# Performance work log

Hardware: AMD Instinct MI355X
Metric: run time of the kernel (lower is better)

Reference implementation:

```python
import jax, jax.numpy as jnp
import numpy as np
from jax import lax

D = 4            # shift radius
NSHIFT = 2 * D + 1  # 9 shifts per axis -> 81 total


def setup_inputs() -> dict:
    key = jax.random.key(0)
    k1, k2, k3, k4, k5, k6 = jax.random.split(key, 6)
    B, C, H, W = 4, 256, 64, 128
    R = 16  # reduction ratio
    feat1 = jax.random.normal(k1, (B, C, H, W), dtype=jnp.float32)
    feat2 = jax.random.normal(k2, (B, C, H, W), dtype=jnp.float32)
    # ca_conv1: Conv2d(C, C//R, 1) -> weight [C//R, C], bias [C//R]
    w1 = jax.random.normal(k3, (C // R, C), dtype=jnp.float32) * (1.0 / np.sqrt(C))
    b1 = jax.random.normal(k4, (C // R,), dtype=jnp.float32) * 0.01
    # ca_conv2: Conv2d(C//R, C, 1) -> weight [C, C//R], bias [C]
    w2 = jax.random.normal(k5, (C, C // R), dtype=jnp.float32) * (1.0 / np.sqrt(C // R))
    b2 = jax.random.normal(k6, (C,), dtype=jnp.float32) * 0.01
    return {"feat1": feat1, "feat2": feat2, "w1": w1, "b1": b1, "w2": w2, "b2": b2}


def reference(feat1, feat2, w1, b1, w2, b2):
    B, C, H, W = feat1.shape
    # zero-pad feat2 spatially by D on each side (matches F.pad constant 0)
    feat2p = jnp.pad(feat2, ((0, 0), (0, 0), (D, D), (D, D)))

    def one_shift(carry, idx):
        i = idx // NSHIFT
        j = idx % NSHIFT
        f2 = lax.dynamic_slice(feat2p, (0, 0, i, j), (B, C, H, W))
        sim = feat1 * f2                              # [B,C,H,W]
        pooled = jnp.mean(sim, axis=(2, 3))           # global avg pool -> [B,C]
        a = pooled @ w1.T + b1                        # [B,C//R] (1x1 conv == matmul)
        a = a @ w2.T + b2                             # [B,C]
        a = jax.nn.sigmoid(a)
        out = jnp.mean(a[:, :, None, None] * sim, axis=1)  # channel mean -> [B,H,W]
        return carry, out

    _, cv = lax.scan(one_shift, None, jnp.arange(NSHIFT * NSHIFT))  # [81,B,H,W]
    return jnp.transpose(cv, (1, 0, 2, 3))  # [B,81,H,W]
```

## Files before the change

### kernel.cpp

```cpp
#include <hip/hip_runtime.h>
#include <math.h>


#define HH 64
#define WW 128
#define CC 256
#define BB 4

__global__ __launch_bounds__(576) void corr_pool_kernel(
    const float* __restrict__ f1, const float* __restrict__ f2,
    float* __restrict__ pooled) {
  const int t  = threadIdx.x;
  const int bc = blockIdx.x;
  const float* f1p = f1 + (size_t)bc * (HH * WW);
  const float* f2p = f2 + (size_t)bc * (HH * WW);

  __shared__ float4 f2s4[72 * 35];

  const float4 z4 = make_float4(0.f, 0.f, 0.f, 0.f);
  for (int u = t; u < 72 * 35; u += 576) {
    const int rl = u / 35, k = u - rl * 35;
    const int gr = rl - 4;
    float4 v = z4;
    if ((unsigned)gr < 64u && k >= 1 && k <= 32)
      v = *(const float4*)(f2p + (gr << 7) + ((k - 1) << 2));
    f2s4[u] = v;
  }
  __syncthreads();

  const int h  = t / 9;
  const int di = t - h * 9;
  const float4* f2row = &f2s4[(h + di) * 35];
  const float* f1row  = f1p + (h << 7);

  float s9[9];
#pragma unroll
  for (int j = 0; j < 9; ++j) s9[j] = 0.f;

  alignas(16) float f1c[16], f2wc[24];
#pragma unroll
  for (int m = 0; m < 4; ++m)
    *(float4*)&f1c[4 * m] = *(const float4*)(f1row + (m << 2));
#pragma unroll
  for (int m = 0; m < 6; ++m) *(float4*)&f2wc[4 * m] = f2row[m];

  for (int seg = 0; seg < 8; ++seg) {
    const int nxt = (seg < 7) ? seg + 1 : 7;
    alignas(16) float f1n[16], f2wn[24];
#pragma unroll
    for (int m = 0; m < 4; ++m)
      *(float4*)&f1n[4 * m] =
          *(const float4*)(f1row + (nxt << 4) + (m << 2));
#pragma unroll
    for (int m = 0; m < 6; ++m) *(float4*)&f2wn[4 * m] = f2row[(nxt << 2) + m];

#pragma unroll
    for (int k = 0; k < 16; ++k) {
      const float a = f1c[k];
#pragma unroll
      for (int j = 0; j < 9; ++j) s9[j] += a * f2wc[k + j];
    }
#pragma unroll
    for (int m = 0; m < 16; ++m) f1c[m] = f1n[m];
#pragma unroll
    for (int m = 0; m < 24; ++m) f2wc[m] = f2wn[m];
  }

  __syncthreads();
  float* red  = (float*)f2s4;
  float* red2 = red + 64 * 81;
#pragma unroll
  for (int j = 0; j < 9; ++j) red[h * 81 + di * 9 + j] = s9[j];
  __syncthreads();

  if (t < 567) {
    const int col = t % 81, g = t / 81;
    const int r0 = g * 9, r1 = (g == 6) ? 64 : r0 + 9;
    float acc = 0.f;
#pragma unroll 3
    for (int rr = r0; rr < r1; ++rr) acc += red[rr * 81 + col];
    red2[g * 81 + col] = acc;
  }
  __syncthreads();

  if (t < 81) {
    float acc = 0.f;
#pragma unroll
    for (int g = 0; g < 7; ++g) acc += red2[g * 81 + t];
    const int b = bc >> 8, c = bc & 255;
    pooled[(size_t)(b * 81 + t) * 256 + c] = acc;
  }
}

__global__ __launch_bounds__(256) void mlp_kernel(
    const float* __restrict__ pooled, const float* __restrict__ w1,
    const float* __restrict__ b1, const float* __restrict__ w2,
    const float* __restrict__ b2, float* __restrict__ At) {
  const int bs = blockIdx.x;
  const int t  = threadIdx.x;
  const int b  = bs / 81;
  const int s  = bs - b * 81;
  __shared__ float p[256];
  __shared__ float hid[16];

  p[t] = pooled[(size_t)bs * 256 + t] * (1.0f / 8192.0f);
  __syncthreads();

  const int g = t >> 4, ln = t & 15;
  float acc = 0.f;
#pragma unroll
  for (int m = 0; m < 16; ++m) {
    const int c = (m << 4) + ln;
    acc += w1[(g << 8) + c] * p[c];
  }
  acc += __shfl_xor(acc, 1);
  acc += __shfl_xor(acc, 2);
  acc += __shfl_xor(acc, 4);
  acc += __shfl_xor(acc, 8);
  if (ln == 0) hid[g] = acc + b1[g];
  __syncthreads();

  float acc2 = b2[t];
#pragma unroll
  for (int k = 0; k < 16; ++k) acc2 += w2[(t << 4) + k] * hid[k];
  const float sv = 1.0f / (1.0f + __expf(-acc2));
  At[((size_t)(b * 256 + t)) * 81 + s] = sv;
}

__device__ __forceinline__ void fma_win(
    const float4 x4, const float4 A4, const float4 B4, const float4 C4,
    const float* __restrict__ coef, const bool vA, const bool vC,
    float acc[9][4]) {
  alignas(16) float f2r[12];
  f2r[0]  = vA ? A4.x : 0.f;
  f2r[1]  = vA ? A4.y : 0.f;
  f2r[2]  = vA ? A4.z : 0.f;
  f2r[3]  = vA ? A4.w : 0.f;
  f2r[4]  = B4.x; f2r[5] = B4.y; f2r[6] = B4.z; f2r[7] = B4.w;
  f2r[8]  = vC ? C4.x : 0.f;
  f2r[9]  = vC ? C4.y : 0.f;
  f2r[10] = vC ? C4.z : 0.f;
  f2r[11] = vC ? C4.w : 0.f;
  alignas(16) const float xx[4] = {x4.x, x4.y, x4.z, x4.w};
#pragma unroll
  for (int j = 0; j < 9; ++j) {
    const float wj = coef[j];
#pragma unroll
    for (int k = 0; k < 4; ++k) acc[j][k] += wj * (xx[k] * f2r[k + j]);
  }
}

__global__ __launch_bounds__(64, 4) void out_kernel(
    const float* __restrict__ f1, const float* __restrict__ f2,
    const float* __restrict__ At, float* __restrict__ out,
    float* __restrict__ part) {
  const int bid  = blockIdx.x;
  const int x    = bid & 7;
  const int q    = bid >> 3;
  const int i    = q % 9;
  const int tq   = q / 9;
  const int tile = tq * 8 + x;
  const int half = tile & 1;
  const int rt   = (tile >> 1) & 31;
  const int b    = tile >> 6;
  const int h0   = rt << 1;

  const int t    = threadIdx.x;
  const int r    = t >> 5;
  const int cidx = t & 31;
  const int w0   = cidx << 2;
  const int h    = h0 + r;
  const int hr   = h + i - 4;
  const bool rowok = ((unsigned)hr < 64u);

  float acc[9][4];
#pragma unroll
  for (int j = 0; j < 9; ++j)
#pragma unroll
    for (int k = 0; k < 4; ++k) acc[j][k] = 0.f;

  if (rowok) {
    const int c0 = half << 7;
    const float* pa1 = f1 + (size_t)b * (CC * 8192) + (size_t)c0 * 8192 +
                       (h << 7) + w0;
    const float* pa2 = f2 + (size_t)b * (CC * 8192) + (size_t)c0 * 8192 +
                       (hr << 7);
    const float* pb1 = pa1 + (size_t)64 * 8192;
    const float* pb2 = pa2 + (size_t)64 * 8192;
    const float* Aa  = At + (size_t)b * (CC * 81) + (size_t)c0 * 81 + i * 9;

    const bool vA  = (cidx > 0);
    const bool vC  = (cidx < 31);
    const int ofsA = vA ? (w0 - 4) : 0;
    const int ofsC = vC ? (w0 + 4) : 120;
    const int CH   = 8192;

    float4 Axa = *(const float4*)(pa1);
    float4 AaA = *(const float4*)(pa2 + ofsA);
    float4 AaB = *(const float4*)(pa2 + w0);
    float4 AaC = *(const float4*)(pa2 + ofsC);
    float4 Axb = *(const float4*)(pb1);
    float4 AbA = *(const float4*)(pb2 + ofsA);
    float4 AbB = *(const float4*)(pb2 + w0);
    float4 AbC = *(const float4*)(pb2 + ofsC);

    for (int c = 0; c < 64; c += 2) {
      pa1 += CH; pa2 += CH; pb1 += CH; pb2 += CH;
      const float4 Bxa = *(const float4*)(pa1);
      const float4 BaA = *(const float4*)(pa2 + ofsA);
      const float4 BaB = *(const float4*)(pa2 + w0);
      const float4 BaC = *(const float4*)(pa2 + ofsC);
      const float4 Bxb = *(const float4*)(pb1);
      const float4 BbA = *(const float4*)(pb2 + ofsA);
      const float4 BbB = *(const float4*)(pb2 + w0);
      const float4 BbC = *(const float4*)(pb2 + ofsC);

      {
        const float* ca = Aa + (size_t)c * 81;
        const float* cb = ca + (size_t)64 * 81;
        fma_win(Axa, AaA, AaB, AaC, ca, vA, vC, acc);
        fma_win(Axb, AbA, AbB, AbC, cb, vA, vC, acc);
      }

      const int adv = (c < 62) ? CH : 0;
      pa1 += adv; pa2 += adv; pb1 += adv; pb2 += adv;
      Axa = *(const float4*)(pa1);
      AaA = *(const float4*)(pa2 + ofsA);
      AaB = *(const float4*)(pa2 + w0);
      AaC = *(const float4*)(pa2 + ofsC);
      Axb = *(const float4*)(pb1);
      AbA = *(const float4*)(pb2 + ofsA);
      AbB = *(const float4*)(pb2 + w0);
      AbC = *(const float4*)(pb2 + ofsC);

      {
        const float* ca = Aa + (size_t)(c + 1) * 81;
        const float* cb = ca + (size_t)64 * 81;
        fma_win(Bxa, BaA, BaB, BaC, ca, vA, vC, acc);
        fma_win(Bxb, BbA, BbB, BbC, cb, vA, vC, acc);
      }
    }
  }

  float* dst = half ? part : out;
  const float inv = 1.0f / 256.0f;
#pragma unroll
  for (int j = 0; j < 9; ++j) {
    float4 o;
    o.x = acc[j][0] * inv;
    o.y = acc[j][1] * inv;
    o.z = acc[j][2] * inv;
    o.w = acc[j][3] * inv;
    *(float4*)(dst + (((size_t)(b * 81 + i * 9 + j) * 64 + h) << 7) + w0) = o;
  }
}

__global__ __launch_bounds__(256) void combine_kernel(
    float* __restrict__ out, const float* __restrict__ part) {
  const size_t idx = (size_t)blockIdx.x * 256 + threadIdx.x;
  float4* o4       = (float4*)out;
  const float4* p4 = (const float4*)part;
  const float4 a = o4[idx], p = p4[idx];
  float4 rv;
  rv.x = a.x + p.x; rv.y = a.y + p.y; rv.z = a.z + p.z; rv.w = a.w + p.w;
  o4[idx] = rv;
}

extern "C" void kernel_launch(void* const* d_in, const int* in_sizes, int n_in,
                              void* d_out, int out_size, void* d_ws, size_t ws_size,
                              hipStream_t stream) {
  const float* feat1 = (const float*)d_in[0];
  const float* feat2 = (const float*)d_in[1];
  const float* w1    = (const float*)d_in[2];
  const float* b1    = (const float*)d_in[3];
  const float* w2    = (const float*)d_in[4];
  const float* b2    = (const float*)d_in[5];
  float* out = (float*)d_out;

  float* pooled = (float*)d_ws;
  float* At     = pooled + 82944;
  float* cpart  = At + 82944;

  corr_pool_kernel<<<1024, 576, 0, stream>>>(feat1, feat2, pooled);
  mlp_kernel<<<4 * 81, 256, 0, stream>>>(pooled, w1, b1, w2, b2, At);
  out_kernel<<<2304, 64, 0, stream>>>(feat1, feat2, At, out, cpart);
  combine_kernel<<<2592, 256, 0, stream>>>(out, cpart);
}
```

Before: 212.6 us.

## Share feat tiles across 9 row-shift waves via async LDS double buffering

The output kernel is restructured so that one 576-thread block (9 waves, one per vertical shift) handles a 2-row tile. Each channel's feat1 rows and the 12 halo rows of feat2 are loaded once into LDS with global_load_lds async copies, double buffered across channels. Previously each of the 9 shift blocks re-read the same feat2 and feat1 data from global memory. The change adds a block barrier per channel iteration and cuts the grid to 256 blocks, which may leave part of the GPU idle.

```diff
diff --git a/kernel.cpp b/kernel.cpp
--- a/kernel.cpp
+++ b/kernel.cpp
@@ -127,51 +127,66 @@
   At[((size_t)(b * 256 + t)) * 81 + s] = sv;
 }
 
-__device__ __forceinline__ void fma_win(
-    const float4 x4, const float4 A4, const float4 B4, const float4 C4,
-    const float* __restrict__ coef, const bool vA, const bool vC,
-    float acc[9][4]) {
-  alignas(16) float f2r[12];
-  f2r[0]  = vA ? A4.x : 0.f;
-  f2r[1]  = vA ? A4.y : 0.f;
-  f2r[2]  = vA ? A4.z : 0.f;
-  f2r[3]  = vA ? A4.w : 0.f;
-  f2r[4]  = B4.x; f2r[5] = B4.y; f2r[6] = B4.z; f2r[7] = B4.w;
-  f2r[8]  = vC ? C4.x : 0.f;
-  f2r[9]  = vC ? C4.y : 0.f;
-  f2r[10] = vC ? C4.z : 0.f;
-  f2r[11] = vC ? C4.w : 0.f;
-  alignas(16) const float xx[4] = {x4.x, x4.y, x4.z, x4.w};
-#pragma unroll
-  for (int j = 0; j < 9; ++j) {
-    const float wj = coef[j];
-#pragma unroll
-    for (int k = 0; k < 4; ++k) acc[j][k] += wj * (xx[k] * f2r[k + j]);
-  }
-}
-
-__global__ __launch_bounds__(64, 4) void out_kernel(
+__device__ __forceinline__ void async16(const float* g, void* lds) {
+  __builtin_amdgcn_global_load_lds(
+      (const __attribute__((address_space(1))) void*)g,
+      (__attribute__((address_space(3))) void*)lds, 16, 0, 0);
+}
+
+__global__ __launch_bounds__(576) void out_kernel(
     const float* __restrict__ f1, const float* __restrict__ f2,
     const float* __restrict__ At, float* __restrict__ out,
     float* __restrict__ part) {
   const int bid  = blockIdx.x;
-  const int x    = bid & 7;
-  const int q    = bid >> 3;
-  const int i    = q % 9;
-  const int tq   = q / 9;
-  const int tile = tq * 8 + x;
-  const int half = tile & 1;
-  const int rt   = (tile >> 1) & 31;
-  const int b    = tile >> 6;
+  const int work = (bid & 7) * 32 + (bid >> 3);
+  const int rt   = work & 31;
+  const int half = (work >> 5) & 1;
+  const int b    = work >> 6;
   const int h0   = rt << 1;
 
   const int t    = threadIdx.x;
-  const int r    = t >> 5;
-  const int cidx = t & 31;
+  const int wv   = t >> 6;
+  const int lane = t & 63;
+  const int r    = lane >> 5;
+  const int cidx = lane & 31;
   const int w0   = cidx << 2;
   const int h    = h0 + r;
-  const int hr   = h + i - 4;
-  const bool rowok = ((unsigned)hr < 64u);
+  const int iu   = __builtin_amdgcn_readfirstlane(wv);
+
+  __shared__ float4 st[2][2][12][32];
+
+  const int c0 = half << 7;
+  const float* f1pl = f1 + ((size_t)b * 256 + c0) * 8192;
+  const float* f2pl = f2 + ((size_t)b * 256 + c0) * 8192;
+  const float* Aa   = At + ((size_t)(b * 256 + c0)) * 81 + iu * 9;
+
+  const int chA   = (wv >= 6) ? 1 : 0;
+  const int slotA = wv - 6 * chA;
+  const bool isF1A = (slotA == 5);
+  const int rowA  = h0 - 4 + 2 * slotA + (lane >> 5);
+  const bool validA = isF1A || ((unsigned)rowA < 64u);
+  const float* gA = (isF1A ? f1pl + h0 * 128
+                           : f2pl + (h0 - 4 + 2 * slotA) * 128)
+                    + (size_t)chA * 8192 + lane * 4;
+
+  const int slotB = ((wv < 3) ? wv : 0) + 3;
+  const bool isF1B = (slotB == 5);
+  const int rowB  = h0 - 4 + 2 * slotB + (lane >> 5);
+  const bool validB = isF1B || ((unsigned)rowB < 64u);
+  const float* gB = (isF1B ? f1pl + h0 * 128
+                           : f2pl + (h0 - 4 + 2 * slotB) * 128)
+                    + (size_t)8192 + lane * 4;
+
+  {
+    const float4 z4 = make_float4(0.f, 0.f, 0.f, 0.f);
+    float4* stf = &st[0][0][0][0];
+    for (int u = t; u < 2 * 2 * 12 * 32; u += 576) stf[u] = z4;
+  }
+  __syncthreads();
+
+  if (validA) async16(gA, &st[0][chA][2 * slotA][0]);
+  if (wv < 3 && validB) async16(gB, &st[0][1][2 * slotB][0]);
+  __syncthreads();
 
   float acc[9][4];
 #pragma unroll
@@ -179,67 +194,51 @@
 #pragma unroll
     for (int k = 0; k < 4; ++k) acc[j][k] = 0.f;
 
-  if (rowok) {
-    const int c0 = half << 7;
-    const float* pa1 = f1 + (size_t)b * (CC * 8192) + (size_t)c0 * 8192 +
-                       (h << 7) + w0;
-    const float* pa2 = f2 + (size_t)b * (CC * 8192) + (size_t)c0 * 8192 +
-                       (hr << 7);
-    const float* pb1 = pa1 + (size_t)64 * 8192;
-    const float* pb2 = pa2 + (size_t)64 * 8192;
-    const float* Aa  = At + (size_t)b * (CC * 81) + (size_t)c0 * 81 + i * 9;
-
-    const bool vA  = (cidx > 0);
-    const bool vC  = (cidx < 31);
-    const int ofsA = vA ? (w0 - 4) : 0;
-    const int ofsC = vC ? (w0 + 4) : 120;
-    const int CH   = 8192;
-
-    float4 Axa = *(const float4*)(pa1);
-    float4 AaA = *(const float4*)(pa2 + ofsA);
-    float4 AaB = *(const float4*)(pa2 + w0);
-    float4 AaC = *(const float4*)(pa2 + ofsC);
-    float4 Axb = *(const float4*)(pb1);
-    float4 AbA = *(const float4*)(pb2 + ofsA);
-    float4 AbB = *(const float4*)(pb2 + w0);
-    float4 AbC = *(const float4*)(pb2 + ofsC);
-
-    for (int c = 0; c < 64; c += 2) {
-      pa1 += CH; pa2 += CH; pb1 += CH; pb2 += CH;
-      const float4 Bxa = *(const float4*)(pa1);
-      const float4 BaA = *(const float4*)(pa2 + ofsA);
-      const float4 BaB = *(const float4*)(pa2 + w0);
-      const float4 BaC = *(const float4*)(pa2 + ofsC);
-      const float4 Bxb = *(const float4*)(pb1);
-      const float4 BbA = *(const float4*)(pb2 + ofsA);
-      const float4 BbB = *(const float4*)(pb2 + w0);
-      const float4 BbC = *(const float4*)(pb2 + ofsC);
-
-      {
-        const float* ca = Aa + (size_t)c * 81;
-        const float* cb = ca + (size_t)64 * 81;
-        fma_win(Axa, AaA, AaB, AaC, ca, vA, vC, acc);
-        fma_win(Axb, AbA, AbB, AbC, cb, vA, vC, acc);
-      }
-
-      const int adv = (c < 62) ? CH : 0;
-      pa1 += adv; pa2 += adv; pb1 += adv; pb2 += adv;
-      Axa = *(const float4*)(pa1);
-      AaA = *(const float4*)(pa2 + ofsA);
-      AaB = *(const float4*)(pa2 + w0);
-      AaC = *(const float4*)(pa2 + ofsC);
-      Axb = *(const float4*)(pb1);
-      AbA = *(const float4*)(pb2 + ofsA);
-      AbB = *(const float4*)(pb2 + w0);
-      AbC = *(const float4*)(pb2 + ofsC);
-
-      {
-        const float* ca = Aa + (size_t)(c + 1) * 81;
-        const float* cb = ca + (size_t)64 * 81;
-        fma_win(Bxa, BaA, BaB, BaC, ca, vA, vC, acc);
-        fma_win(Bxb, BbA, BbB, BbC, cb, vA, vC, acc);
+  const bool vA = (cidx > 0);
+  const bool vC = (cidx < 31);
+  const int cxm1 = vA ? cidx - 1 : cidx;
+  const int cxp1 = vC ? cidx + 1 : cidx;
+  const int riu  = r + iu;
+
+  for (int k = 0; k < 64; ++k) {
+    const int cur = k & 1, nxt = cur ^ 1;
+
+    const int adv = (k < 63) ? 16384 : 0;
+    gA += adv; gB += adv;
+    if (validA) async16(gA, &st[nxt][chA][2 * slotA][0]);
+    if (wv < 3 && validB) async16(gB, &st[nxt][1][2 * slotB][0]);
+
+    const float* ca = Aa + (size_t)(2 * k) * 81;
+#pragma unroll
+    for (int sub = 0; sub < 2; ++sub) {
+      const float* cf = ca + sub * 81;
+      const float4 x4 = st[cur][sub][10 + r][cidx];
+      const float4 A4 = st[cur][sub][riu][cxm1];
+      const float4 B4 = st[cur][sub][riu][cidx];
+      const float4 C4 = st[cur][sub][riu][cxp1];
+
+      alignas(16) float f2r[12];
+      f2r[0]  = vA ? A4.x : 0.f;
+      f2r[1]  = vA ? A4.y : 0.f;
+      f2r[2]  = vA ? A4.z : 0.f;
+      f2r[3]  = vA ? A4.w : 0.f;
+      f2r[4]  = B4.x; f2r[5] = B4.y; f2r[6] = B4.z; f2r[7] = B4.w;
+      f2r[8]  = vC ? C4.x : 0.f;
+      f2r[9]  = vC ? C4.y : 0.f;
+      f2r[10] = vC ? C4.z : 0.f;
+      f2r[11] = vC ? C4.w : 0.f;
+      alignas(16) const float xx[4] = {x4.x, x4.y, x4.z, x4.w};
+
+#pragma unroll
+      for (int j = 0; j < 9; ++j) {
+        const float wj = cf[j];
+#pragma unroll
+        for (int kk = 0; kk < 4; ++kk)
+          acc[j][kk] += wj * (xx[kk] * f2r[kk + j]);
       }
     }
+
+    __syncthreads();
   }
 
   float* dst = half ? part : out;
@@ -251,7 +250,7 @@
     o.y = acc[j][1] * inv;
     o.z = acc[j][2] * inv;
     o.w = acc[j][3] * inv;
-    *(float4*)(dst + (((size_t)(b * 81 + i * 9 + j) * 64 + h) << 7) + w0) = o;
+    *(float4*)(dst + (((size_t)(b * 81 + iu * 9 + j) * 64 + h) << 7) + w0) = o;
   }
 }
 
@@ -283,6 +282,6 @@
 
   corr_pool_kernel<<<1024, 576, 0, stream>>>(feat1, feat2, pooled);
   mlp_kernel<<<4 * 81, 256, 0, stream>>>(pooled, w1, b1, w2, b2, At);
-  out_kernel<<<2304, 64, 0, stream>>>(feat1, feat2, At, out, cpart);
+  out_kernel<<<256, 576, 0, stream>>>(feat1, feat2, At, out, cpart);
   combine_kernel<<<2592, 256, 0, stream>>>(out, cpart);
 }
```

Result: faster. 193.0 us (-9.2%).
